# Kernel tuning notes

Hardware: AMD Instinct MI355X
Metric: run time of the kernel (lower is better)

## Reference

```python
import jax, jax.numpy as jnp
import numpy as np

EPS = 1e-5  # torch LayerNorm default

def setup_inputs() -> dict:
    key = jax.random.key(0)
    k1, k2, k3 = jax.random.split(key, 3)
    x = jax.random.normal(k1, (8, 256, 256, 256), dtype=jnp.float32)
    w_size = 256
    bound = 1.0 / np.sqrt(w_size)
    W = jax.random.uniform(k2, (w_size, w_size), dtype=jnp.float32, minval=-bound, maxval=bound)
    b = jax.random.uniform(k3, (w_size,), dtype=jnp.float32, minval=-bound, maxval=bound)
    return {"x": x, "W": W, "b": b}

def reference(x, W, b):
    # x: [B, 2C, G, Wd]; chunk along channel dim
    u, v = jnp.split(x, 2, axis=1)
    # LayerNorm over all non-batch dims (weight=1, bias=0 since module is
    # constructed fresh inside forward)
    mean = jnp.mean(v, axis=(1, 2, 3), keepdims=True)
    var = jnp.mean(jnp.square(v - mean), axis=(1, 2, 3), keepdims=True)
    v = (v - mean) * jax.lax.rsqrt(var + EPS)
    # Linear along last dim: y = v @ W.T + b
    v = jnp.einsum('bcgw,ow->bcgo', v, W) + b
    return u * (v + 1.0)
```

## Files before the change

### kernel.cpp

```cpp
#include <hip/hip_runtime.h>
#include <hip/hip_bf16.h>

typedef __attribute__((ext_vector_type(8))) short short8_t;
typedef __attribute__((ext_vector_type(4))) float f32x4;

__device__ __forceinline__ short f2bf(float f) {
    union { float f; unsigned u; } v; v.f = f;
    unsigned r = (v.u + 0x7FFFu + ((v.u >> 16) & 1u)) >> 16;
    return (short)r;
}

#define N_PER_BATCH 8388608.0f
#define LDW 264

__global__ __launch_bounds__(256) void stats_partial(const float* __restrict__ x,
                                                     float2* __restrict__ partials) {
    int bid = blockIdx.x;
    int batch = bid >> 8;
    int blk   = bid & 255;
    const float* base = x + ((size_t)batch << 24) + (1u << 23) + ((size_t)blk << 15);
    int tid = threadIdx.x;
    float s1 = 0.f, s2 = 0.f;
    #pragma unroll
    for (int i = 0; i < 32; ++i) {
        float4 v = *reinterpret_cast<const float4*>(base + (size_t)(i * 256 + tid) * 4);
        s1 += v.x + v.y + v.z + v.w;
        s2 += v.x * v.x + v.y * v.y + v.z * v.z + v.w * v.w;
    }
    #pragma unroll
    for (int off = 32; off; off >>= 1) {
        s1 += __shfl_down(s1, off);
        s2 += __shfl_down(s2, off);
    }
    __shared__ float2 red[4];
    if ((tid & 63) == 0) red[tid >> 6] = make_float2(s1, s2);
    __syncthreads();
    if (tid == 0) {
        float a1 = 0.f, a2 = 0.f;
        #pragma unroll
        for (int w = 0; w < 4; ++w) { a1 += red[w].x; a2 += red[w].y; }
        partials[bid] = make_float2(a1, a2);
    }
}

__global__ __launch_bounds__(256) void stats_final(const float2* __restrict__ partials,
                                                   float2* __restrict__ stats) {
    int batch = blockIdx.x;
    int tid = threadIdx.x;
    float2 p = partials[(batch << 8) + tid];
    float s1 = p.x, s2 = p.y;
    #pragma unroll
    for (int off = 32; off; off >>= 1) {
        s1 += __shfl_down(s1, off);
        s2 += __shfl_down(s2, off);
    }
    __shared__ float2 red[4];
    if ((tid & 63) == 0) red[tid >> 6] = make_float2(s1, s2);
    __syncthreads();
    if (tid == 0) {
        float a1 = 0.f, a2 = 0.f;
        #pragma unroll
        for (int w = 0; w < 4; ++w) { a1 += red[w].x; a2 += red[w].y; }
        float mean = a1 / N_PER_BATCH;
        float var  = a2 / N_PER_BATCH - mean * mean;
        stats[batch] = make_float2(mean, rsqrtf(var + 1e-5f));
    }
}

__global__ __launch_bounds__(1024, 4) void fused_gemm(const float* __restrict__ x,
                                                      const float* __restrict__ W,
                                                      const float* __restrict__ bias,
                                                      const float2* __restrict__ stats,
                                                      float* __restrict__ out) {
    __shared__ short Wlds[256 * LDW];
    int tid = threadIdx.x;

    #pragma unroll
    for (int i = 0; i < 16; ++i) {
        int idx4 = tid + (i << 10);
        int row = idx4 >> 6;
        int c0  = (idx4 & 63) << 2;
        float4 w4 = reinterpret_cast<const float4*>(W)[idx4];
        short4 s;
        s.x = f2bf(w4.x); s.y = f2bf(w4.y); s.z = f2bf(w4.z); s.w = f2bf(w4.w);
        *reinterpret_cast<short4*>(&Wlds[row * LDW + c0]) = s;
    }
    __syncthreads();

    int wid  = tid >> 6;
    int lane = tid & 63;
    int l15  = lane & 15;
    int l4   = lane >> 4;

    int gw = (blockIdx.x << 4) + wid;
    const int nTiles = 16384;

    for (int tile = gw; tile < nTiles; tile += 4096) {
        int row0 = tile << 4;
        int b_i  = row0 >> 15;
        int cg0  = row0 & 32767;
        const float* vbase = x + ((size_t)b_i << 24) + (1u << 23) + ((size_t)cg0 << 8);
        const float* ubase = x + ((size_t)b_i << 24) + ((size_t)cg0 << 8);
        float*       obase = out + ((size_t)row0 << 8);
        float2 ms = stats[b_i];
        float mean = ms.x, rstd = ms.y;

        short8_t af[8];
        const float* arow = vbase + (size_t)l15 * 256 + (l4 << 3);
        #pragma unroll
        for (int kb = 0; kb < 8; ++kb) {
            float4 p0 = *reinterpret_cast<const float4*>(arow + kb * 32);
            float4 p1 = *reinterpret_cast<const float4*>(arow + kb * 32 + 4);
            short8_t a;
            a[0] = f2bf((p0.x - mean) * rstd);
            a[1] = f2bf((p0.y - mean) * rstd);
            a[2] = f2bf((p0.z - mean) * rstd);
            a[3] = f2bf((p0.w - mean) * rstd);
            a[4] = f2bf((p1.x - mean) * rstd);
            a[5] = f2bf((p1.y - mean) * rstd);
            a[6] = f2bf((p1.z - mean) * rstd);
            a[7] = f2bf((p1.w - mean) * rstd);
            af[kb] = a;
        }

        #pragma unroll 2
        for (int nc = 0; nc < 16; ++nc) {
            int col = (nc << 4) + l15;
            const short* wrow = &Wlds[col * LDW + (l4 << 3)];
            f32x4 acc = {0.f, 0.f, 0.f, 0.f};
            #pragma unroll
            for (int kb = 0; kb < 8; ++kb) {
                short8_t bf = *reinterpret_cast<const short8_t*>(wrow + kb * 32);
                acc = __builtin_amdgcn_mfma_f32_16x16x32_bf16(af[kb], bf, acc, 0, 0, 0);
            }
            float bp1 = bias[col] + 1.0f;
            int rbase = l4 << 2;
            #pragma unroll
            for (int r = 0; r < 4; ++r) {
                int off = ((rbase + r) << 8) + col;
                float uv = ubase[off];
                obase[off] = uv * (acc[r] + bp1);
            }
        }
    }
}

extern "C" void kernel_launch(void* const* d_in, const int* in_sizes, int n_in,
                              void* d_out, int out_size, void* d_ws, size_t ws_size,
                              hipStream_t stream) {
    const float* x    = (const float*)d_in[0];
    const float* W    = (const float*)d_in[1];
    const float* bias = (const float*)d_in[2];
    float* out = (float*)d_out;

    float2* partials = (float2*)d_ws;
    float2* stats    = (float2*)((char*)d_ws + 16384);

    stats_partial<<<2048, 256, 0, stream>>>(x, partials);
    stats_final<<<8, 256, 0, stream>>>(partials, stats);
    fused_gemm<<<256, 1024, 0, stream>>>(x, W, bias, stats, out);
}
```

Baseline: 225.9 us.

## Keep W fragments in registers and stream normalized v tiles through double-buffered LDS

The fused GEMM now has each wave hold a 16-column slice of W as bf16 MFMA fragments in registers, instead of staging all of W in LDS. Each block walks 64 consecutive 16-row tiles of v, normalizing them into a double-buffered LDS tile that all 16 waves share. The MFMA result is transposed within lanes using xor shuffles, so u loads and output stores become float4-wide accesses. The aim is to cut LDS footprint and W re-reads and to vectorize global memory traffic, at the cost of a block-wide barrier on every tile and a fixed mapping of 32 blocks per batch.

```diff
diff --git a/kernel.cpp b/kernel.cpp
--- a/kernel.cpp
+++ b/kernel.cpp
@@ -11,7 +11,7 @@
 }
 
 #define N_PER_BATCH 8388608.0f
-#define LDW 264
+#define LDR 264
 
 __global__ __launch_bounds__(256) void stats_partial(const float* __restrict__ x,
                                                      float2* __restrict__ partials) {
@@ -72,76 +72,100 @@
                                                       const float* __restrict__ bias,
                                                       const float2* __restrict__ stats,
                                                       float* __restrict__ out) {
-    __shared__ short Wlds[256 * LDW];
-    int tid = threadIdx.x;
+    __shared__ short vt[2][16 * LDR];
+    const int tid  = threadIdx.x;
+    const int wid  = tid >> 6;
+    const int lane = tid & 63;
+    const int l15  = lane & 15;
+    const int l4   = lane >> 4;
+    const int q    = l15 & 3;
+    const int qg   = l15 >> 2;
 
-    #pragma unroll
-    for (int i = 0; i < 16; ++i) {
-        int idx4 = tid + (i << 10);
-        int row = idx4 >> 6;
-        int c0  = (idx4 & 63) << 2;
-        float4 w4 = reinterpret_cast<const float4*>(W)[idx4];
+    const int bi = blockIdx.x >> 5;
+    const float2 ms = stats[bi];
+    const float mean = ms.x, rstd = ms.y;
+
+    short8_t bfrag[8];
+    {
+        const float* wbase = W + (size_t)(wid * 16 + l15) * 256 + (l4 << 3);
+        #pragma unroll
+        for (int kb = 0; kb < 8; ++kb) {
+            float4 p0 = *reinterpret_cast<const float4*>(wbase + kb * 32);
+            float4 p1 = *reinterpret_cast<const float4*>(wbase + kb * 32 + 4);
+            short8_t s;
+            s[0] = f2bf(p0.x); s[1] = f2bf(p0.y); s[2] = f2bf(p0.z); s[3] = f2bf(p0.w);
+            s[4] = f2bf(p1.x); s[5] = f2bf(p1.y); s[6] = f2bf(p1.z); s[7] = f2bf(p1.w);
+            bfrag[kb] = s;
+        }
+    }
+    float4 bq = *reinterpret_cast<const float4*>(bias + wid * 16 + (qg << 2));
+    bq.x += 1.f; bq.y += 1.f; bq.z += 1.f; bq.w += 1.f;
+
+    const size_t row0 = (size_t)blockIdx.x << 10;
+    const float* vbase = x + ((size_t)bi << 24) + (1u << 23) + ((row0 & 32767) << 8);
+    const float* ubase = x + ((size_t)bi << 24) + ((row0 & 32767) << 8);
+    float*       obase = out + (row0 << 8);
+
+    const int   srow = tid >> 6;
+    const int   scol = (tid & 63) << 2;
+    const size_t goff = (size_t)srow * 256 + scol;
+    const int   lds_w = srow * LDR + scol;
+
+    const size_t eoff = (size_t)(l4 * 4 + q) * 256 + wid * 16 + (qg << 2);
+
+    const int aoff = l15 * LDR + (l4 << 3);
+
+    {
+        float4 v0 = *reinterpret_cast<const float4*>(vbase + goff);
         short4 s;
-        s.x = f2bf(w4.x); s.y = f2bf(w4.y); s.z = f2bf(w4.z); s.w = f2bf(w4.w);
-        *reinterpret_cast<short4*>(&Wlds[row * LDW + c0]) = s;
+        s.x = f2bf((v0.x - mean) * rstd); s.y = f2bf((v0.y - mean) * rstd);
+        s.z = f2bf((v0.z - mean) * rstd); s.w = f2bf((v0.w - mean) * rstd);
+        *reinterpret_cast<short4*>(&vt[0][lds_w]) = s;
     }
     __syncthreads();
 
-    int wid  = tid >> 6;
-    int lane = tid & 63;
-    int l15  = lane & 15;
-    int l4   = lane >> 4;
+    for (int t = 0; t < 64; ++t) {
+        const int cur = t & 1;
+        const int tn = (t < 63) ? t + 1 : 63;
+        float4 vn = *reinterpret_cast<const float4*>(vbase + ((size_t)tn << 12) + goff);
+        const size_t uo = ((size_t)t << 12) + eoff;
+        float4 u4 = *reinterpret_cast<const float4*>(ubase + uo);
 
-    int gw = (blockIdx.x << 4) + wid;
-    const int nTiles = 16384;
-
-    for (int tile = gw; tile < nTiles; tile += 4096) {
-        int row0 = tile << 4;
-        int b_i  = row0 >> 15;
-        int cg0  = row0 & 32767;
-        const float* vbase = x + ((size_t)b_i << 24) + (1u << 23) + ((size_t)cg0 << 8);
-        const float* ubase = x + ((size_t)b_i << 24) + ((size_t)cg0 << 8);
-        float*       obase = out + ((size_t)row0 << 8);
-        float2 ms = stats[b_i];
-        float mean = ms.x, rstd = ms.y;
-
-        short8_t af[8];
-        const float* arow = vbase + (size_t)l15 * 256 + (l4 << 3);
+        f32x4 acc = {0.f, 0.f, 0.f, 0.f};
         #pragma unroll
         for (int kb = 0; kb < 8; ++kb) {
-            float4 p0 = *reinterpret_cast<const float4*>(arow + kb * 32);
-            float4 p1 = *reinterpret_cast<const float4*>(arow + kb * 32 + 4);
-            short8_t a;
-            a[0] = f2bf((p0.x - mean) * rstd);
-            a[1] = f2bf((p0.y - mean) * rstd);
-            a[2] = f2bf((p0.z - mean) * rstd);
-            a[3] = f2bf((p0.w - mean) * rstd);
-            a[4] = f2bf((p1.x - mean) * rstd);
-            a[5] = f2bf((p1.y - mean) * rstd);
-            a[6] = f2bf((p1.z - mean) * rstd);
-            a[7] = f2bf((p1.w - mean) * rstd);
-            af[kb] = a;
+            short8_t a = *reinterpret_cast<const short8_t*>(&vt[cur][aoff + kb * 32]);
+            acc = __builtin_amdgcn_mfma_f32_16x16x32_bf16(a, bfrag[kb], acc, 0, 0, 0);
         }
 
-        #pragma unroll 2
-        for (int nc = 0; nc < 16; ++nc) {
-            int col = (nc << 4) + l15;
-            const short* wrow = &Wlds[col * LDW + (l4 << 3)];
-            f32x4 acc = {0.f, 0.f, 0.f, 0.f};
-            #pragma unroll
-            for (int kb = 0; kb < 8; ++kb) {
-                short8_t bf = *reinterpret_cast<const short8_t*>(wrow + kb * 32);
-                acc = __builtin_amdgcn_mfma_f32_16x16x32_bf16(af[kb], bf, acc, 0, 0, 0);
-            }
-            float bp1 = bias[col] + 1.0f;
-            int rbase = l4 << 2;
-            #pragma unroll
-            for (int r = 0; r < 4; ++r) {
-                int off = ((rbase + r) << 8) + col;
-                float uv = ubase[off];
-                obase[off] = uv * (acc[r] + bp1);
-            }
-        }
+        float v0 = acc[0], v1 = acc[1], v2 = acc[2], v3 = acc[3];
+        float s0 = __shfl_xor(v1, 1), s1 = __shfl_xor(v0, 1);
+        float s2 = __shfl_xor(v3, 1), s3 = __shfl_xor(v2, 1);
+        const bool qb0 = (q & 1);
+        float w0 = qb0 ? s0 : v0;
+        float w1 = qb0 ? v1 : s1;
+        float w2 = qb0 ? s2 : v2;
+        float w3 = qb0 ? v3 : s3;
+        float t0 = __shfl_xor(w2, 2), t1 = __shfl_xor(w3, 2);
+        float t2 = __shfl_xor(w0, 2), t3 = __shfl_xor(w1, 2);
+        const bool qb1 = (q & 2);
+        float x0 = qb1 ? t0 : w0;
+        float x1 = qb1 ? t1 : w1;
+        float x2 = qb1 ? w2 : t2;
+        float x3 = qb1 ? w3 : t3;
+
+        float4 o;
+        o.x = u4.x * (x0 + bq.x);
+        o.y = u4.y * (x1 + bq.y);
+        o.z = u4.z * (x2 + bq.z);
+        o.w = u4.w * (x3 + bq.w);
+        *reinterpret_cast<float4*>(obase + uo) = o;
+
+        short4 sn;
+        sn.x = f2bf((vn.x - mean) * rstd); sn.y = f2bf((vn.y - mean) * rstd);
+        sn.z = f2bf((vn.z - mean) * rstd); sn.w = f2bf((vn.w - mean) * rstd);
+        *reinterpret_cast<short4*>(&vt[cur ^ 1][lds_w]) = sn;
+        __syncthreads();
     }
 }
 
```

Result: faster. 215.7 us (-4.5%).

## Vectorize epilogue via lane transpose, swizzle W in LDS, prefetch u

Applied to the files above, without the earlier changes.

The epilogue now transposes the 4x4 MFMA accumulator fragments across lanes with xor shuffles, so each lane loads u and stores the output as float4 instead of four scalar strided accesses. The unpadded LDS copy of W uses an XOR swizzle to avoid bank conflicts, and bias+1 is staged in LDS. The u values for the next column chunk are prefetched one iteration ahead, and tiles are visited in reverse order with a fixed trip count of four. The cost is extra shuffle instructions and register pressure, and the launch-bounds occupancy hint is dropped.

```diff
diff --git a/kernel.cpp b/kernel.cpp
--- a/kernel.cpp
+++ b/kernel.cpp
@@ -11,7 +11,6 @@
 }
 
 #define N_PER_BATCH 8388608.0f
-#define LDW 264
 
 __global__ __launch_bounds__(256) void stats_partial(const float* __restrict__ x,
                                                      float2* __restrict__ partials) {
@@ -67,50 +66,62 @@
     }
 }
 
-__global__ __launch_bounds__(1024, 4) void fused_gemm(const float* __restrict__ x,
-                                                      const float* __restrict__ W,
-                                                      const float* __restrict__ bias,
-                                                      const float2* __restrict__ stats,
-                                                      float* __restrict__ out) {
-    __shared__ short Wlds[256 * LDW];
-    int tid = threadIdx.x;
+__global__ __launch_bounds__(1024) void fused_gemm(const float* __restrict__ x,
+                                                   const float* __restrict__ W,
+                                                   const float* __restrict__ bias,
+                                                   const float2* __restrict__ stats,
+                                                   float* __restrict__ out) {
+    __shared__ short wl[65536];
+    __shared__ float bp1[256];
+    const int tid  = threadIdx.x;
+    const int wid  = tid >> 6;
+    const int lane = tid & 63;
+    const int l15  = lane & 15;
+    const int l4   = lane >> 4;
+    const int q    = l15 & 3;
+    const int qg   = l15 >> 2;
 
     #pragma unroll
     for (int i = 0; i < 16; ++i) {
-        int idx4 = tid + (i << 10);
-        int row = idx4 >> 6;
-        int c0  = (idx4 & 63) << 2;
-        float4 w4 = reinterpret_cast<const float4*>(W)[idx4];
+        int idx = tid + (i << 10);
+        int row = idx >> 6;
+        int c0  = (idx & 63) << 2;
+        float4 w4 = reinterpret_cast<const float4*>(W)[idx];
         short4 s;
         s.x = f2bf(w4.x); s.y = f2bf(w4.y); s.z = f2bf(w4.z); s.w = f2bf(w4.w);
-        *reinterpret_cast<short4*>(&Wlds[row * LDW + c0]) = s;
+        int sw = (row << 8) + (c0 ^ ((row & 7) << 3));
+        *reinterpret_cast<short4*>(&wl[sw]) = s;
+    }
+    if (tid < 64) {
+        float4 b4 = reinterpret_cast<const float4*>(bias)[tid];
+        bp1[tid * 4 + 0] = b4.x + 1.f;
+        bp1[tid * 4 + 1] = b4.y + 1.f;
+        bp1[tid * 4 + 2] = b4.z + 1.f;
+        bp1[tid * 4 + 3] = b4.w + 1.f;
     }
     __syncthreads();
 
-    int wid  = tid >> 6;
-    int lane = tid & 63;
-    int l15  = lane & 15;
-    int l4   = lane >> 4;
+    const int gw  = (blockIdx.x << 4) + wid;
+    const int xsw = (l15 & 7) << 3;
 
-    int gw = (blockIdx.x << 4) + wid;
-    const int nTiles = 16384;
+    for (int it = 0; it < 4; ++it) {
+        const int tile = 16383 - gw - (it << 12);
+        const size_t row0 = (size_t)tile << 4;
+        const int bi = (int)(row0 >> 15);
+        const size_t rowb = row0 & 32767;
+        const float2 ms = stats[bi];
+        const float mean = ms.x, rstd = ms.y;
 
-    for (int tile = gw; tile < nTiles; tile += 4096) {
-        int row0 = tile << 4;
-        int b_i  = row0 >> 15;
-        int cg0  = row0 & 32767;
-        const float* vbase = x + ((size_t)b_i << 24) + (1u << 23) + ((size_t)cg0 << 8);
-        const float* ubase = x + ((size_t)b_i << 24) + ((size_t)cg0 << 8);
-        float*       obase = out + ((size_t)row0 << 8);
-        float2 ms = stats[b_i];
-        float mean = ms.x, rstd = ms.y;
+        const float* vrow  = x + ((size_t)bi << 24) + (1u << 23) + (rowb << 8)
+                               + (size_t)l15 * 256 + (l4 << 3);
+        const float* ubase = x + ((size_t)bi << 24) + (rowb << 8);
+        float*       obase = out + (row0 << 8);
 
         short8_t af[8];
-        const float* arow = vbase + (size_t)l15 * 256 + (l4 << 3);
         #pragma unroll
         for (int kb = 0; kb < 8; ++kb) {
-            float4 p0 = *reinterpret_cast<const float4*>(arow + kb * 32);
-            float4 p1 = *reinterpret_cast<const float4*>(arow + kb * 32 + 4);
+            float4 p0 = *reinterpret_cast<const float4*>(vrow + kb * 32);
+            float4 p1 = *reinterpret_cast<const float4*>(vrow + kb * 32 + 4);
             short8_t a;
             a[0] = f2bf((p0.x - mean) * rstd);
             a[1] = f2bf((p0.y - mean) * rstd);
@@ -123,24 +134,49 @@
             af[kb] = a;
         }
 
+        const size_t eo0 = (size_t)(l4 * 4 + q) * 256 + (qg << 2);
+
+        float4 u4 = *reinterpret_cast<const float4*>(ubase + eo0);
+
         #pragma unroll 2
         for (int nc = 0; nc < 16; ++nc) {
-            int col = (nc << 4) + l15;
-            const short* wrow = &Wlds[col * LDW + (l4 << 3)];
+            const int ncn = (nc < 15) ? nc + 1 : 15;
+            float4 u_next = *reinterpret_cast<const float4*>(ubase + eo0 + (ncn << 4));
+
+            const int wb = ((nc << 4) + l15) << 8;
             f32x4 acc = {0.f, 0.f, 0.f, 0.f};
             #pragma unroll
             for (int kb = 0; kb < 8; ++kb) {
-                short8_t bf = *reinterpret_cast<const short8_t*>(wrow + kb * 32);
-                acc = __builtin_amdgcn_mfma_f32_16x16x32_bf16(af[kb], bf, acc, 0, 0, 0);
+                const int off = wb + ((((kb << 5) + (l4 << 3)) ^ xsw));
+                short8_t b = *reinterpret_cast<const short8_t*>(&wl[off]);
+                acc = __builtin_amdgcn_mfma_f32_16x16x32_bf16(af[kb], b, acc, 0, 0, 0);
             }
-            float bp1 = bias[col] + 1.0f;
-            int rbase = l4 << 2;
-            #pragma unroll
-            for (int r = 0; r < 4; ++r) {
-                int off = ((rbase + r) << 8) + col;
-                float uv = ubase[off];
-                obase[off] = uv * (acc[r] + bp1);
-            }
+
+            float a0 = acc[0], a1 = acc[1], a2 = acc[2], a3 = acc[3];
+            float s0 = __shfl_xor(a1, 1), s1 = __shfl_xor(a0, 1);
+            float s2 = __shfl_xor(a3, 1), s3 = __shfl_xor(a2, 1);
+            const bool qb0 = (q & 1);
+            float w0 = qb0 ? s0 : a0;
+            float w1 = qb0 ? a1 : s1;
+            float w2 = qb0 ? s2 : a2;
+            float w3 = qb0 ? a3 : s3;
+            float t0 = __shfl_xor(w2, 2), t1 = __shfl_xor(w3, 2);
+            float t2 = __shfl_xor(w0, 2), t3 = __shfl_xor(w1, 2);
+            const bool qb1 = (q & 2);
+            float x0 = qb1 ? t0 : w0;
+            float x1 = qb1 ? t1 : w1;
+            float x2 = qb1 ? w2 : t2;
+            float x3 = qb1 ? w3 : t3;
+
+            float4 bq = *reinterpret_cast<const float4*>(&bp1[(nc << 4) + (qg << 2)]);
+            const size_t uo = eo0 + (nc << 4);
+            float4 o;
+            o.x = u4.x * (x0 + bq.x);
+            o.y = u4.y * (x1 + bq.y);
+            o.z = u4.z * (x2 + bq.z);
+            o.w = u4.w * (x3 + bq.w);
+            *reinterpret_cast<float4*>(obase + uo) = o;
+            u4 = u_next;
         }
     }
 }
```

After: 220.2 us. 1.03x faster.
